# Kernel tuning notes

Measured on AMD Instinct MI355X. Metric: run time of the kernel, lower is better.

The kernel has to match this reference:

```python
import jax, jax.numpy as jnp
import numpy as np

C = 384        # channels
T_KERNEL = 121 # self.t, temporal kernel support
T_SIM = 65536  # simulated samples
SIZE = 2       # batch of simulations
BLOCK = 512    # overlap-add FFT block size (fast length >= T_KERNEL)


def _oa_conv_dewhiten(noise, spatial_std, vt_spatial, kernel_fft, s2):
    """Overlap-add FFT filtering (single_inv_oaconv1d, norm='ortho') then
    spatial dewhitening einsum, as in StationaryFactorizedNoise.simulate."""
    N, t_padded = noise.shape
    block_size = 2 * (kernel_fft.shape[0] - 1)
    t_out = t_padded - s2 + 1              # valid-conv output length
    hop = block_size - s2 + 1              # overlap-add segment length
    nb = -(-t_padded // hop)               # ceil division
    pad = nb * hop - t_padded
    x = jnp.pad(noise, ((0, 0), (0, pad))).reshape(N, nb, hop)
    xf = jnp.fft.rfft(x, n=block_size, axis=-1, norm='ortho')
    # kernel_fft is real (sqrt of mean power spectrum)
    yb = jnp.fft.irfft(xf * kernel_fft, n=block_size, axis=-1, norm='ortho')
    L = nb * hop + (block_size - hop)
    idx = (jnp.arange(nb)[:, None] * hop + jnp.arange(block_size)[None, :]).reshape(-1)
    y = jnp.zeros((N, L), noise.dtype).at[:, idx].add(yb.reshape(N, -1))
    y = y[:, s2 - 1: s2 - 1 + t_out]       # valid part of the convolution
    c = spatial_std.shape[0]
    noise3 = y.reshape(N // c, c, t_out)   # (size, c, t)
    spatial_part = spatial_std[:, None] * vt_spatial  # (c, d)
    return jnp.einsum('nct,cd->ntd', noise3, spatial_part)


def setup_inputs() -> dict:
    key = jax.random.key(0)
    k1, k2, k3, k4 = jax.random.split(key, 4)
    t_padded = T_SIM + T_KERNEL - 1
    return {
        'noise': jax.random.normal(k1, (SIZE * C, t_padded), dtype=jnp.float32),
        'spatial_std': jax.random.uniform(k2, (C,), dtype=jnp.float32, minval=0.5, maxval=1.5),
        'vt_spatial': jax.random.normal(k3, (C, C), dtype=jnp.float32) / np.sqrt(C),
        'kernel_fft': jax.random.uniform(k4, (BLOCK // 2 + 1,), dtype=jnp.float32, minval=0.1, maxval=1.0),
        's2': T_KERNEL,
    }


def reference(noise, spatial_std, vt_spatial, kernel_fft, s2):
    return _oa_conv_dewhiten(noise, spatial_std, vt_spatial, kernel_fft, s2)
```

## Files before the change

kernel.cpp:

```cpp
#include <hip/hip_runtime.h>
#include <hip/hip_bf16.h>

#define TPAD   65656
#define TOUT   65536
#define CCH    384
#define NROWS  768
#define HOP    392
#define NB     168
#define BS     512
#define KPAD   416
#define M1     129024
#define M2     131072

typedef __attribute__((ext_vector_type(8))) _Float16 f16x8;
typedef __attribute__((ext_vector_type(4))) _Float16 f16x4;
typedef __attribute__((ext_vector_type(4))) float    f32x4;
typedef __attribute__((ext_vector_type(8))) float    f32x8;

__device__ __forceinline__ void gload_lds16(const void* g, void* l) {
    __builtin_amdgcn_global_load_lds(
        (__attribute__((address_space(1))) void*)g,
        (__attribute__((address_space(3))) void*)l, 16, 0, 0);
}

__global__ void build_h_kernel(const float* __restrict__ kfft, float* __restrict__ h) {
    __shared__ float Ks[257];
    int j = threadIdx.x;
    if (j < 257) Ks[j] = kfft[j];
    __syncthreads();
    float acc = Ks[0] + ((j & 1) ? -Ks[256] : Ks[256]);
    const float w0 = 6.2831853071795864769f / 512.0f;
    for (int f = 1; f < 256; ++f) {
        int m = (f * j) & 511;
        acc += 2.0f * Ks[f] * cosf(w0 * (float)m);
    }
    h[j] = acc * (1.0f / 512.0f);
}

__global__ void build_ht_kernel(const float* __restrict__ h, _Float16* __restrict__ Ht) {
    int j = blockIdx.x;
    int i = blockIdx.y * 256 + threadIdx.x;
    if (i >= KPAD) return;
    float v = (i < HOP) ? h[(j - i) & 511] : 0.0f;
    Ht[j * KPAD + i] = (_Float16)v;
}

__global__ void build_spt_kernel(const float* __restrict__ sstd, const float* __restrict__ vt,
                                 _Float16* __restrict__ spT) {
    int d = blockIdx.x;
    int c = threadIdx.x;
    spT[d * CCH + c] = (_Float16)(sstd[c] * vt[c * CCH + d]);
}

__global__ __launch_bounds__(256) void cast_kernel(const float* __restrict__ noise,
                                                   _Float16* __restrict__ A16) {
    int gid = blockIdx.x * 256 + threadIdx.x;
    int row = gid / 52;
    int seg = gid - row * 52;
    int i0  = seg * 8;
    int r   = row / NB;
    int b   = row - r * NB;
    int lim = (b == NB - 1) ? (TPAD - (NB - 1) * HOP) : HOP;
    f16x8 o = {};
    if (i0 + 8 <= lim) {
        const float* src = noise + r * TPAD + b * HOP + i0;
        f32x4 v0 = *(const f32x4*)src;
        f32x4 v1 = *(const f32x4*)(src + 4);
        f32x8 v = {v0.x, v0.y, v0.z, v0.w, v1.x, v1.y, v1.z, v1.w};
        o = __builtin_convertvector(v, f16x8);
    }
    *(f16x8*)(A16 + row * KPAD + i0) = o;
}

__global__ __launch_bounds__(256) void gemm1_kernel(const _Float16* __restrict__ A16,
                                                    const _Float16* __restrict__ Ht,
                                                    _Float16* __restrict__ yb) {
    __shared__ __align__(16) _Float16 As[128 * 32];
    __shared__ __align__(16) _Float16 Bs[128 * 32];
    const int tid  = threadIdx.x;
    const int w    = tid >> 6, lane = tid & 63;
    const int quad = lane >> 4, lm = lane & 15;
    const int wm   = w >> 1, wn = w & 1;
    const int m0   = blockIdx.y * 128;
    const int n0   = blockIdx.x * 128;

    f32x4 acc[4][4] = {};

    for (int kt = 0; kt < KPAD / 32; ++kt) {
        const int k0 = kt * 32;
#pragma unroll
        for (int ro = 0; ro < 2; ++ro) {
            int gidx = ro * 256 + tid;
            int row  = gidx >> 2;
            int col  = (gidx & 3) * 8;
            gload_lds16(A16 + (size_t)(m0 + row) * KPAD + k0 + col,
                        As + (ro * 256 + (tid & ~63)) * 8);
            gload_lds16(Ht + (n0 + row) * KPAD + k0 + col,
                        Bs + (ro * 256 + (tid & ~63)) * 8);
        }
        __syncthreads();

        f16x8 a[4], b[4];
#pragma unroll
        for (int mi = 0; mi < 4; ++mi)
            a[mi] = *(const f16x8*)(As + (wm * 64 + mi * 16 + lm) * 32 + quad * 8);
#pragma unroll
        for (int ni = 0; ni < 4; ++ni)
            b[ni] = *(const f16x8*)(Bs + (wn * 64 + ni * 16 + lm) * 32 + quad * 8);
#pragma unroll
        for (int mi = 0; mi < 4; ++mi)
#pragma unroll
            for (int ni = 0; ni < 4; ++ni)
                acc[mi][ni] = __builtin_amdgcn_mfma_f32_16x16x32_f16(a[mi], b[ni], acc[mi][ni], 0, 0, 0);
        __syncthreads();
    }

#pragma unroll
    for (int mi = 0; mi < 4; ++mi)
#pragma unroll
        for (int e = 0; e < 4; ++e) {
            int row = m0 + wm * 64 + mi * 16 + quad * 4 + e;
            _Float16* dst = yb + (size_t)row * BS + n0 + wn * 64 + lm;
#pragma unroll
            for (int ni = 0; ni < 4; ++ni)
                dst[ni * 16] = (_Float16)acc[mi][ni][e];
        }
}

__global__ __launch_bounds__(256) void oa_kernel(const _Float16* __restrict__ yb,
                                                 _Float16* __restrict__ Yt) {
    __shared__ float Ls[32][33];
    const int tx = threadIdx.x & 31, ty = threadIdx.x >> 5;
    const int t0 = blockIdx.x * 32, c0 = blockIdx.y * 32, n = blockIdx.z;
#pragma unroll
    for (int s = 0; s < 4; ++s) {
        int cc = ty + s * 8;
        int r  = n * CCH + c0 + cc;
        int g  = t0 + tx + 120;
        int b  = g / HOP;
        int j  = g - b * HOP;
        int idx = (r * NB + b) * BS + j;
        float v = (float)yb[idx];
        if (j < 120) v += (float)yb[idx - 120];
        Ls[cc][tx] = v;
    }
    __syncthreads();
#pragma unroll
    for (int s = 0; s < 4; ++s) {
        int tt = ty + s * 8;
        Yt[((size_t)n * TOUT + t0 + tt) * CCH + c0 + tx] = (_Float16)Ls[tx][tt];
    }
}

__global__ __launch_bounds__(256) void gemm2_kernel(const _Float16* __restrict__ Yt,
                                                    const _Float16* __restrict__ spT,
                                                    float* __restrict__ outp) {
    __shared__ __align__(16) _Float16 As[128 * 32];
    __shared__ __align__(16) _Float16 Bs[128 * 32];
    const int tid  = threadIdx.x;
    const int w    = tid >> 6, lane = tid & 63;
    const int quad = lane >> 4, lm = lane & 15;
    const int wm   = w >> 1, wn = w & 1;
    const int m0   = blockIdx.y * 128;
    const int n0   = blockIdx.x * 128;

    f32x4 acc[4][4] = {};

    for (int kt = 0; kt < CCH / 32; ++kt) {
        const int k0 = kt * 32;
#pragma unroll
        for (int ro = 0; ro < 2; ++ro) {
            int gidx = ro * 256 + tid;
            int row  = gidx >> 2;
            int col  = (gidx & 3) * 8;
            gload_lds16(Yt + (size_t)(m0 + row) * CCH + k0 + col,
                        As + (ro * 256 + (tid & ~63)) * 8);
            gload_lds16(spT + (n0 + row) * CCH + k0 + col,
                        Bs + (ro * 256 + (tid & ~63)) * 8);
        }
        __syncthreads();

        f16x8 a[4], b[4];
#pragma unroll
        for (int mi = 0; mi < 4; ++mi)
            a[mi] = *(const f16x8*)(As + (wm * 64 + mi * 16 + lm) * 32 + quad * 8);
#pragma unroll
        for (int ni = 0; ni < 4; ++ni)
            b[ni] = *(const f16x8*)(Bs + (wn * 64 + ni * 16 + lm) * 32 + quad * 8);
#pragma unroll
        for (int mi = 0; mi < 4; ++mi)
#pragma unroll
            for (int ni = 0; ni < 4; ++ni)
                acc[mi][ni] = __builtin_amdgcn_mfma_f32_16x16x32_f16(a[mi], b[ni], acc[mi][ni], 0, 0, 0);
        __syncthreads();
    }

#pragma unroll
    for (int mi = 0; mi < 4; ++mi)
#pragma unroll
        for (int e = 0; e < 4; ++e) {
            int row = m0 + wm * 64 + mi * 16 + quad * 4 + e;
            float* dst = outp + (size_t)row * CCH + n0 + wn * 64 + lm;
#pragma unroll
            for (int ni = 0; ni < 4; ++ni)
                dst[ni * 16] = acc[mi][ni][e];
        }
}

extern "C" void kernel_launch(void* const* d_in, const int* in_sizes, int n_in,
                              void* d_out, int out_size, void* d_ws, size_t ws_size,
                              hipStream_t stream) {
    const float* noise = (const float*)d_in[0];
    const float* sstd  = (const float*)d_in[1];
    const float* vt    = (const float*)d_in[2];
    const float* kfft  = (const float*)d_in[3];
    float* out = (float*)d_out;

    char* ws = (char*)d_ws;
    float*    h   = (float*)ws;
    _Float16* Ht  = (_Float16*)(ws + 2048);
    _Float16* spT = (_Float16*)(ws + 428032);
    _Float16* yb  = (_Float16*)(ws + 722944);
    _Float16* Yt  = (_Float16*)(ws + 132843520);
    _Float16* A16 = (_Float16*)(ws + 233506816);

    build_h_kernel  <<<1, 512, 0, stream>>>(kfft, h);
    build_ht_kernel <<<dim3(512, 2), 256, 0, stream>>>(h, Ht);
    build_spt_kernel<<<CCH, CCH, 0, stream>>>(sstd, vt, spT);

    cast_kernel <<<M1 * 52 / 256, 256, 0, stream>>>(noise, A16);
    gemm1_kernel<<<dim3(BS / 128, M1 / 128), 256, 0, stream>>>(A16, Ht, yb);
    oa_kernel   <<<dim3(TOUT / 32, CCH / 32, 2), 256, 0, stream>>>(yb, Yt);
    gemm2_kernel<<<dim3(CCH / 128, M2 / 128), 256, 0, stream>>>(Yt, spT, out);
}
```

Baseline: 668.8 us.

## Fuse fp32-to-fp16 cast into GEMM1 A loads, vectorize stores, swizzle block order

Removes the separate cast kernel and the fp16 A staging buffer: gemm1 now reads fp32 noise directly with per-row bounds, converts in registers and writes to LDS, prefetching the next K-slice during the MFMA loop. The gemm1 epilogue writes 4 halves per lane in a permuted column layout, and oa_kernel un-permutes through permcol. Both GEMMs remap block IDs to group blocks with related tiles together for cache locality. The cost is more register pressure and a non-async A load path in gemm1.

```diff
diff --git a/kernel.cpp b/kernel.cpp
--- a/kernel.cpp
+++ b/kernel.cpp
@@ -52,53 +52,66 @@
     spT[d * CCH + c] = (_Float16)(sstd[c] * vt[c * CCH + d]);
 }
 
-__global__ __launch_bounds__(256) void cast_kernel(const float* __restrict__ noise,
-                                                   _Float16* __restrict__ A16) {
-    int gid = blockIdx.x * 256 + threadIdx.x;
-    int row = gid / 52;
-    int seg = gid - row * 52;
-    int i0  = seg * 8;
-    int r   = row / NB;
-    int b   = row - r * NB;
-    int lim = (b == NB - 1) ? (TPAD - (NB - 1) * HOP) : HOP;
-    f16x8 o = {};
-    if (i0 + 8 <= lim) {
-        const float* src = noise + r * TPAD + b * HOP + i0;
-        f32x4 v0 = *(const f32x4*)src;
-        f32x4 v1 = *(const f32x4*)(src + 4);
-        f32x8 v = {v0.x, v0.y, v0.z, v0.w, v1.x, v1.y, v1.z, v1.w};
-        o = __builtin_convertvector(v, f16x8);
-    }
-    *(f16x8*)(A16 + row * KPAD + i0) = o;
-}
-
-__global__ __launch_bounds__(256) void gemm1_kernel(const _Float16* __restrict__ A16,
+__global__ __launch_bounds__(256) void gemm1_kernel(const float* __restrict__ noise,
                                                     const _Float16* __restrict__ Ht,
                                                     _Float16* __restrict__ yb) {
     __shared__ __align__(16) _Float16 As[128 * 32];
     __shared__ __align__(16) _Float16 Bs[128 * 32];
     const int tid  = threadIdx.x;
-    const int w    = tid >> 6, lane = tid & 63;
+    const int lane = tid & 63;
+    const int w    = tid >> 6;
     const int quad = lane >> 4, lm = lane & 15;
     const int wm   = w >> 1, wn = w & 1;
-    const int m0   = blockIdx.y * 128;
-    const int n0   = blockIdx.x * 128;
+
+    const int bid = blockIdx.x + (blockIdx.y << 2);
+    const int lid = (bid & 7) * 504 + (bid >> 3);
+    const int n0  = (lid & 3) * 128;
+    const int m0  = (lid >> 2) * 128;
+
+    const int colseg = (tid & 3) * 8;
+    const int arow0  = tid >> 2;
+    const float* asrc0; const float* asrc1;
+    int alim0, alim1;
+    {
+        int m = m0 + arow0;
+        int r = m / NB, b = m - r * NB;
+        asrc0 = noise + (size_t)r * TPAD + b * HOP;
+        alim0 = (b == NB - 1) ? (TPAD - (NB - 1) * HOP) : HOP;
+        m = m0 + arow0 + 64;
+        r = m / NB; b = m - r * NB;
+        asrc1 = noise + (size_t)r * TPAD + b * HOP;
+        alim1 = (b == NB - 1) ? (TPAD - (NB - 1) * HOP) : HOP;
+    }
+
+    f32x4 pv00, pv01, pv10, pv11;
+#define LOADA(K0) {                                                           \
+        int i0 = (K0) + colseg;                                               \
+        if (i0 < alim0) { pv00 = *(const f32x4*)(asrc0 + i0);                 \
+                          pv01 = *(const f32x4*)(asrc0 + i0 + 4); }           \
+        else            { pv00 = (f32x4){}; pv01 = (f32x4){}; }               \
+        if (i0 < alim1) { pv10 = *(const f32x4*)(asrc1 + i0);                 \
+                          pv11 = *(const f32x4*)(asrc1 + i0 + 4); }           \
+        else            { pv10 = (f32x4){}; pv11 = (f32x4){}; }               \
+    }
+
+    LOADA(0);
 
     f32x4 acc[4][4] = {};
 
     for (int kt = 0; kt < KPAD / 32; ++kt) {
         const int k0 = kt * 32;
-#pragma unroll
-        for (int ro = 0; ro < 2; ++ro) {
-            int gidx = ro * 256 + tid;
-            int row  = gidx >> 2;
-            int col  = (gidx & 3) * 8;
-            gload_lds16(A16 + (size_t)(m0 + row) * KPAD + k0 + col,
-                        As + (ro * 256 + (tid & ~63)) * 8);
-            gload_lds16(Ht + (n0 + row) * KPAD + k0 + col,
-                        Bs + (ro * 256 + (tid & ~63)) * 8);
-        }
-        __syncthreads();
+        gload_lds16(Ht + (n0 + arow0) * KPAD + k0 + colseg,
+                    Bs + (tid & ~63) * 8);
+        gload_lds16(Ht + (n0 + arow0 + 64) * KPAD + k0 + colseg,
+                    Bs + (256 + (tid & ~63)) * 8);
+        {
+            f32x8 v0 = {pv00.x, pv00.y, pv00.z, pv00.w, pv01.x, pv01.y, pv01.z, pv01.w};
+            *(f16x8*)(As + arow0 * 32 + colseg) = __builtin_convertvector(v0, f16x8);
+            f32x8 v1 = {pv10.x, pv10.y, pv10.z, pv10.w, pv11.x, pv11.y, pv11.z, pv11.w};
+            *(f16x8*)(As + (arow0 + 64) * 32 + colseg) = __builtin_convertvector(v1, f16x8);
+        }
+        __syncthreads();
+        if (kt + 1 < KPAD / 32) { LOADA(k0 + 32); }
 
         f16x8 a[4], b[4];
 #pragma unroll
@@ -114,17 +127,21 @@
                 acc[mi][ni] = __builtin_amdgcn_mfma_f32_16x16x32_f16(a[mi], b[ni], acc[mi][ni], 0, 0, 0);
         __syncthreads();
     }
+#undef LOADA
 
 #pragma unroll
     for (int mi = 0; mi < 4; ++mi)
 #pragma unroll
         for (int e = 0; e < 4; ++e) {
             int row = m0 + wm * 64 + mi * 16 + quad * 4 + e;
-            _Float16* dst = yb + (size_t)row * BS + n0 + wn * 64 + lm;
-#pragma unroll
-            for (int ni = 0; ni < 4; ++ni)
-                dst[ni * 16] = (_Float16)acc[mi][ni][e];
-        }
+            f16x4 o = {(_Float16)acc[mi][0][e], (_Float16)acc[mi][1][e],
+                       (_Float16)acc[mi][2][e], (_Float16)acc[mi][3][e]};
+            *(f16x4*)(yb + (size_t)row * BS + n0 + wn * 64 + lm * 4) = o;
+        }
+}
+
+__device__ __forceinline__ int permcol(int j) {
+    return (j & ~63) | ((j & 15) << 2) | ((j >> 4) & 3);
 }
 
 __global__ __launch_bounds__(256) void oa_kernel(const _Float16* __restrict__ yb,
@@ -139,9 +156,9 @@
         int g  = t0 + tx + 120;
         int b  = g / HOP;
         int j  = g - b * HOP;
-        int idx = (r * NB + b) * BS + j;
-        float v = (float)yb[idx];
-        if (j < 120) v += (float)yb[idx - 120];
+        size_t base = (size_t)(r * NB + b) * BS;
+        float v = (float)yb[base + permcol(j)];
+        if (j < 120) v += (float)yb[base - BS + permcol(j + 392)];
         Ls[cc][tx] = v;
     }
     __syncthreads();
@@ -161,8 +178,11 @@
     const int w    = tid >> 6, lane = tid & 63;
     const int quad = lane >> 4, lm = lane & 15;
     const int wm   = w >> 1, wn = w & 1;
-    const int m0   = blockIdx.y * 128;
-    const int n0   = blockIdx.x * 128;
+
+    const int bid = blockIdx.x + blockIdx.y * 3;
+    const int lid = (bid & 7) * 384 + (bid >> 3);
+    const int n0  = (lid % 3) * 128;
+    const int m0  = (lid / 3) * 128;
 
     f32x4 acc[4][4] = {};
 
@@ -222,14 +242,12 @@
     _Float16* spT = (_Float16*)(ws + 428032);
     _Float16* yb  = (_Float16*)(ws + 722944);
     _Float16* Yt  = (_Float16*)(ws + 132843520);
-    _Float16* A16 = (_Float16*)(ws + 233506816);
 
     build_h_kernel  <<<1, 512, 0, stream>>>(kfft, h);
     build_ht_kernel <<<dim3(512, 2), 256, 0, stream>>>(h, Ht);
     build_spt_kernel<<<CCH, CCH, 0, stream>>>(sstd, vt, spT);
 
-    cast_kernel <<<M1 * 52 / 256, 256, 0, stream>>>(noise, A16);
-    gemm1_kernel<<<dim3(BS / 128, M1 / 128), 256, 0, stream>>>(A16, Ht, yb);
+    gemm1_kernel<<<dim3(BS / 128, M1 / 128), 256, 0, stream>>>(noise, Ht, yb);
     oa_kernel   <<<dim3(TOUT / 32, CCH / 32, 2), 256, 0, stream>>>(yb, Yt);
     gemm2_kernel<<<dim3(CCH / 128, M2 / 128), 256, 0, stream>>>(Yt, spT, out);
 }
```

After: 639.4 us. -4.4%, faster.
